# Kernel optimization log

Measured on AMD Instinct MI355X. Metric: run time of the kernel, lower is better.

The kernel has to match this reference:

```python
import jax, jax.numpy as jnp
import numpy as np

B, S, D = 4, 2048, 1024
H = 16
HD = D // H          # 64
HALF = HD // 2       # 32


def _rope(t, cos, sin):
    # t: [B, S, H, HD]; cos/sin: [S, HALF]
    tr = t.reshape(*t.shape[:-1], HALF, 2)
    t0, t1 = tr[..., 0], tr[..., 1]
    c = cos[None, :, None, :]
    s = sin[None, :, None, :]
    out = jnp.stack([t0 * c - t1 * s, t0 * s + t1 * c], axis=-1)
    return out.reshape(t.shape)


def setup_inputs() -> dict:
    key = jax.random.key(0)
    ks = jax.random.split(key, 7)
    x = jax.random.normal(ks[0], (B, S, D), dtype=jnp.float32)
    # rotary tables (theta=10000 convention)
    inv_freq = 1.0 / (10000.0 ** (np.arange(0, HD, 2, dtype=np.float32) / HD))
    angles = np.arange(S, dtype=np.float32)[:, None] * inv_freq[None, :]
    freqs_cos = jnp.asarray(np.cos(angles))
    freqs_sin = jnp.asarray(np.sin(angles))
    scale = 1.0 / np.sqrt(D)
    wq = jax.random.normal(ks[1], (D, D), dtype=jnp.float32) * scale
    wk = jax.random.normal(ks[2], (D, D), dtype=jnp.float32) * scale
    wv = jax.random.normal(ks[3], (D, D), dtype=jnp.float32) * scale
    wo = jax.random.normal(ks[4], (D, D), dtype=jnp.float32) * scale
    return {"x": x, "freqs_cos": freqs_cos, "freqs_sin": freqs_sin,
            "wq": wq, "wk": wk, "wv": wv, "wo": wo}


def reference(x, freqs_cos, freqs_sin, wq, wk, wv, wo):
    b, s, d = x.shape
    q = (x @ wq.T).reshape(b, s, H, HD)
    k = (x @ wk.T).reshape(b, s, H, HD)
    v = (x @ wv.T).reshape(b, s, H, HD)
    q = _rope(q, freqs_cos, freqs_sin)
    k = _rope(k, freqs_cos, freqs_sin)
    # [B, H, S, HD]
    q = q.transpose(0, 2, 1, 3)
    k = k.transpose(0, 2, 1, 3)
    v = v.transpose(0, 2, 1, 3)
    scores = jnp.einsum("bhqd,bhkd->bhqk", q, k) / jnp.sqrt(jnp.float32(HD))
    causal = jnp.tril(jnp.ones((s, s), dtype=bool))
    scores = jnp.where(causal[None, None, :, :], scores, jnp.finfo(scores.dtype).min)
    attn = jax.nn.softmax(scores, axis=-1)
    out = jnp.einsum("bhqk,bhkd->bhqd", attn, v)
    out = out.transpose(0, 2, 1, 3).reshape(b, s, d)
    return out @ wo.T
```

## Files before the change

### kernel.cpp

```cpp
#include <hip/hip_runtime.h>
#include <hip/hip_bf16.h>
#include <cstdint>
#include <cstddef>

#define BB 4
#define SS 2048
#define DD 1024
#define HH 16
#define HDD 64

typedef __bf16 bf16_t;
typedef __bf16 bf16x8 __attribute__((ext_vector_type(8)));
typedef float f32x4 __attribute__((ext_vector_type(4)));
typedef unsigned u32x2 __attribute__((ext_vector_type(2)));

__device__ __forceinline__ unsigned short f2bf(float f) {
    unsigned u = __float_as_uint(f);
    unsigned r = (u + 0x7FFFu + ((u >> 16) & 1u)) >> 16;
    return (unsigned short)r;
}
__device__ __forceinline__ bf16_t f2bf16(float f) {
    return __builtin_bit_cast(bf16_t, f2bf(f));
}
__device__ __forceinline__ bf16x8 cvt8(float4 a, float4 b) {
    bf16x8 r;
    r[0] = f2bf16(a.x); r[1] = f2bf16(a.y);
    r[2] = f2bf16(a.z); r[3] = f2bf16(a.w);
    r[4] = f2bf16(b.x); r[5] = f2bf16(b.y);
    r[6] = f2bf16(b.z); r[7] = f2bf16(b.w);
    return r;
}
__device__ __forceinline__ unsigned cvtpk_bf16(float lo, float hi) {
    unsigned r;
    asm("v_cvt_pk_bf16_f32 %0, %1, %2" : "=v"(r) : "v"(lo), "v"(hi));
    return r;
}
__device__ __forceinline__ float exp2_raw(float x) {
    float r;
    asm("v_exp_f32 %0, %1" : "=v"(r) : "v"(x));
    return r;
}

#define GLL16(gp, lp)                                                          \
    __builtin_amdgcn_global_load_lds(                                          \
        (const __attribute__((address_space(1))) void*)(gp),                   \
        (__attribute__((address_space(3))) void*)(lp), 16, 0, 0)

__global__ __launch_bounds__(256) void cvt1(const float* __restrict__ in,
                                            bf16_t* __restrict__ out) {
    size_t i = (size_t)blockIdx.x * 256 + threadIdx.x;
    const float4* p = (const float4*)in + i * 2;
    *(bf16x8*)(out + i * 8) = cvt8(p[0], p[1]);
}
__global__ __launch_bounds__(256) void cvt4(
    const float* __restrict__ w0, const float* __restrict__ w1,
    const float* __restrict__ w2, const float* __restrict__ w3,
    bf16_t* __restrict__ o0, bf16_t* __restrict__ o1,
    bf16_t* __restrict__ o2, bf16_t* __restrict__ o3) {
    const float* in = blockIdx.y == 0 ? w0 : blockIdx.y == 1 ? w1
                    : blockIdx.y == 2 ? w2 : w3;
    bf16_t* out = blockIdx.y == 0 ? o0 : blockIdx.y == 1 ? o1
                : blockIdx.y == 2 ? o2 : o3;
    size_t i = (size_t)blockIdx.x * 256 + threadIdx.x;
    const float4* p = (const float4*)in + i * 2;
    *(bf16x8*)(out + i * 8) = cvt8(p[0], p[1]);
}

__global__ __launch_bounds__(256, 2) void gemm_qkv(
    const bf16_t* __restrict__ A, const bf16_t* __restrict__ Wall,
    bf16_t* __restrict__ Qb, bf16_t* __restrict__ Kb,
    bf16_t* __restrict__ Vt,
    const float* __restrict__ fcos, const float* __restrict__ fsin,
    float qscale)
{
    constexpr int K = 1024;
    __shared__ alignas(16) bf16_t lA[128 * 64];
    __shared__ alignas(16) bf16_t lB[128 * 64];

    const int tid  = threadIdx.x;
    const int w    = tid >> 6;
    const int lane = tid & 63;
    const int quad = lane >> 4;
    const int l16  = lane & 15;
    const int wm   = w >> 1;
    const int wn   = w & 1;
    const int m0   = blockIdx.y * 128;
    const int n0   = blockIdx.x * 128;
    const int sub  = n0 >> 10;

    f32x4 acc[4][4];
#pragma unroll
    for (int i = 0; i < 4; i++)
#pragma unroll
        for (int j = 0; j < 4; j++) acc[i][j] = (f32x4){0.f, 0.f, 0.f, 0.f};

    const int srow8 = lane >> 3;
    const int slot  = lane & 7;

    for (int k0 = 0; k0 < K; k0 += 64) {
#pragma unroll
        for (int i = 0; i < 4; ++i) {
            int row = w * 32 + i * 8;
            GLL16(A + (size_t)(m0 + row + srow8) * K + k0 + slot * 8,
                  &lA[row * 64]);
            GLL16(Wall + (size_t)(n0 + row + srow8) * K + k0 + slot * 8,
                  &lB[row * 64]);
        }
        __syncthreads();
#pragma unroll
        for (int kk = 0; kk < 2; ++kk) {
            bf16x8 af[4], bfr[4];
#pragma unroll
            for (int mt = 0; mt < 4; ++mt)
                af[mt] = *(const bf16x8*)
                    &lA[(wm * 64 + mt * 16 + l16) * 64 + (kk * 4 + quad) * 8];
#pragma unroll
            for (int nt = 0; nt < 4; ++nt)
                bfr[nt] = *(const bf16x8*)
                    &lB[(wn * 64 + nt * 16 + l16) * 64 + (kk * 4 + quad) * 8];
#pragma unroll
            for (int mt = 0; mt < 4; ++mt)
#pragma unroll
                for (int nt = 0; nt < 4; ++nt)
                    acc[mt][nt] = __builtin_amdgcn_mfma_f32_16x16x32_bf16(
                        af[mt], bfr[nt], acc[mt][nt], 0, 0, 0);
        }
        __syncthreads();
    }

    if (sub < 2) {
        unsigned short* Cu = (unsigned short*)(sub == 0 ? Qb : Kb);
        const float scale = sub == 0 ? qscale : 1.0f;
#pragma unroll
        for (int mt = 0; mt < 4; ++mt) {
#pragma unroll
            for (int nt = 0; nt < 4; ++nt) {
                int col  = (n0 & 1023) + wn * 64 + nt * 16 + l16;
                int h    = col >> 6;
                int d    = col & 63;
                int pidx = d >> 1;
                bool even = (col & 1) == 0;
#pragma unroll
                for (int r = 0; r < 4; ++r) {
                    int m = m0 + wm * 64 + mt * 16 + quad * 4 + r;
                    int b = m >> 11;
                    int s = m & 2047;
                    float v  = acc[mt][nt][r];
                    float p  = __shfl_xor(v, 1);
                    float c  = fcos[s * 32 + pidx];
                    float sn = fsin[s * 32 + pidx];
                    float o  = even ? (v * c - p * sn) : (p * sn + v * c);
                    Cu[(size_t)((b * HH + h) * SS + s) * HDD + d] =
                        f2bf(o * scale);
                }
            }
        }
    } else {
        unsigned short* Cu = (unsigned short*)Vt;
#pragma unroll
        for (int mt = 0; mt < 4; ++mt) {
#pragma unroll
            for (int nt = 0; nt < 4; ++nt) {
                int col = (n0 & 1023) + wn * 64 + nt * 16 + l16;
                int h = col >> 6, d = col & 63;
#pragma unroll
                for (int r = 0; r < 4; ++r) {
                    int m = m0 + wm * 64 + mt * 16 + quad * 4 + r;
                    int b = m >> 11, s = m & 2047;
                    Cu[(size_t)((b * HH + h) * HDD + d) * SS + s] =
                        f2bf(acc[mt][nt][r]);
                }
            }
        }
    }
}

__global__ __launch_bounds__(256, 2) void gemm_out(
    const bf16_t* __restrict__ A, const bf16_t* __restrict__ W,
    float* __restrict__ Cf)
{
    constexpr int K = 1024, N = 1024;
    __shared__ alignas(16) bf16_t lA[128 * 64];
    __shared__ alignas(16) bf16_t lB[128 * 64];

    const int tid  = threadIdx.x;
    const int w    = tid >> 6;
    const int lane = tid & 63;
    const int quad = lane >> 4;
    const int l16  = lane & 15;
    const int wm   = w >> 1;
    const int wn   = w & 1;
    const int m0   = blockIdx.y * 128;
    const int n0   = blockIdx.x * 128;

    f32x4 acc[4][4];
#pragma unroll
    for (int i = 0; i < 4; i++)
#pragma unroll
        for (int j = 0; j < 4; j++) acc[i][j] = (f32x4){0.f, 0.f, 0.f, 0.f};

    const int srow8 = lane >> 3;
    const int slot  = lane & 7;

    for (int k0 = 0; k0 < K; k0 += 64) {
#pragma unroll
        for (int i = 0; i < 4; ++i) {
            int row = w * 32 + i * 8;
            GLL16(A + (size_t)(m0 + row + srow8) * K + k0 + slot * 8,
                  &lA[row * 64]);
            GLL16(W + (size_t)(n0 + row + srow8) * K + k0 + slot * 8,
                  &lB[row * 64]);
        }
        __syncthreads();
#pragma unroll
        for (int kk = 0; kk < 2; ++kk) {
            bf16x8 af[4], bfr[4];
#pragma unroll
            for (int mt = 0; mt < 4; ++mt)
                af[mt] = *(const bf16x8*)
                    &lA[(wm * 64 + mt * 16 + l16) * 64 + (kk * 4 + quad) * 8];
#pragma unroll
            for (int nt = 0; nt < 4; ++nt)
                bfr[nt] = *(const bf16x8*)
                    &lB[(wn * 64 + nt * 16 + l16) * 64 + (kk * 4 + quad) * 8];
#pragma unroll
            for (int mt = 0; mt < 4; ++mt)
#pragma unroll
                for (int nt = 0; nt < 4; ++nt)
                    acc[mt][nt] = __builtin_amdgcn_mfma_f32_16x16x32_bf16(
                        af[mt], bfr[nt], acc[mt][nt], 0, 0, 0);
        }
        __syncthreads();
    }

#pragma unroll
    for (int mt = 0; mt < 4; ++mt) {
        int mrow = m0 + wm * 64 + mt * 16 + quad * 4;
#pragma unroll
        for (int nt = 0; nt < 4; ++nt) {
            int col = n0 + wn * 64 + nt * 16 + l16;
#pragma unroll
            for (int r = 0; r < 4; ++r)
                Cf[(size_t)(mrow + r) * N + col] = acc[mt][nt][r];
        }
    }
}

__global__ __launch_bounds__(256, 2) void attn(
    const bf16_t* __restrict__ Q, const bf16_t* __restrict__ Kt,
    const bf16_t* __restrict__ Vt, bf16_t* __restrict__ O)
{
    __shared__ alignas(16) bf16_t lK[128 * 64];
    __shared__ alignas(16) bf16_t lV[64 * 128];

    const int tid  = threadIdx.x;
    const int w    = tid >> 6;
    const int lane = tid & 63;
    const int quad = lane >> 4;
    const int l16  = lane & 15;

    const int blk  = blockIdx.x;
    const int xcd  = blk & 7;
    const int rest = blk >> 3;
    const int j    = rest & 15;
    const int bh   = ((rest >> 4) << 3) | xcd;
    const int T    = (j & 1) ? (j >> 1) : (15 - (j >> 1));

    const int b = bh >> 4, h = bh & 15;
    unsigned short* Ou = (unsigned short*)O;
    const bf16_t* Qb = Q  + (size_t)bh * SS * HDD;
    const bf16_t* Kb = Kt + (size_t)bh * SS * HDD;
    const bf16_t* Vb = Vt + (size_t)bh * HDD * SS;

    const int q0 = T * 128 + w * 32;
    const int nt128 = T + 1;

    const int krow_l = lane >> 3;
    const int kchk   = lane & 7;
    const int vrow_l = lane >> 4;
    const int vchk   = lane & 15;

    auto stage = [&](int kb2) {
#pragma unroll
        for (int i = 0; i < 4; ++i) {
            int row = w * 32 + i * 8 + krow_l;
            GLL16(Kb + (size_t)(kb2 + row) * HDD + ((kchk ^ (row & 7)) * 8),
                  &lK[(w * 32 + i * 8) * 64]);
        }
#pragma unroll
        for (int i = 0; i < 4; ++i) {
            int row = w * 16 + i * 4 + vrow_l;
            GLL16(Vb + (size_t)row * SS + kb2 + ((vchk ^ (row & 7)) * 8),
                  &lV[(w * 16 + i * 4) * 128]);
        }
    };

    bf16x8 qf[2][2];
#pragma unroll
    for (int qs = 0; qs < 2; ++qs) {
        const bf16_t* qp =
            Qb + (size_t)(q0 + qs * 16 + l16) * HDD + quad * 8;
        qf[qs][0] = *(const bf16x8*)(qp);
        qf[qs][1] = *(const bf16x8*)(qp + 32);
    }

    f32x4 o[2][4];
    float ps[2];
#pragma unroll
    for (int qs = 0; qs < 2; ++qs) {
        ps[qs] = 0.f;
#pragma unroll
        for (int i = 0; i < 4; ++i) o[qs][i] = (f32x4){0.f, 0.f, 0.f, 0.f};
    }

    for (int t = 0; t < nt128; ++t) {
        const int kb2 = t * 128;
        stage(kb2);
        __syncthreads();

        for (int p = 0; p < 2; ++p) {
            const int kbp = kb2 + p * 64;
            if (kbp < q0 + 32) {
                const bool diag = (kbp + 63 > q0);

                bf16x8 kf[4][2];
#pragma unroll
                for (int nt = 0; nt < 4; ++nt) {
                    const int row = p * 64 + nt * 16 + l16;
#pragma unroll
                    for (int hf = 0; hf < 2; ++hf)
                        kf[nt][hf] = *(const bf16x8*)
                            &lK[row * 64 + (((hf * 4 + quad) ^ (row & 7)) * 8)];
                }
                bf16x8 vf[2][4];
#pragma unroll
                for (int kk = 0; kk < 2; ++kk)
#pragma unroll
                    for (int nt = 0; nt < 4; ++nt) {
                        const int row = nt * 16 + l16;
                        vf[kk][nt] = *(const bf16x8*)
                            &lV[row * 128 +
                                ((p * 8 + ((kk * 4 + quad) ^ (row & 7))) * 8)];
                    }

                unsigned pk[4][2][2];
#pragma unroll
                for (int nt = 0; nt < 4; ++nt) {
                    const int krow = kbp + nt * 16 + quad * 4;
#pragma unroll
                    for (int qs = 0; qs < 2; ++qs) {
                        f32x4 s = (f32x4){0.f, 0.f, 0.f, 0.f};
                        s = __builtin_amdgcn_mfma_f32_16x16x32_bf16(
                            kf[nt][0], qf[qs][0], s, 0, 0, 0);
                        s = __builtin_amdgcn_mfma_f32_16x16x32_bf16(
                            kf[nt][1], qf[qs][1], s, 0, 0, 0);
                        if (diag) {
                            const int qcol = q0 + qs * 16 + l16;
#pragma unroll
                            for (int r = 0; r < 4; ++r)
                                if (krow + r > qcol) s[r] = -1e30f;
                        }
                        float ev[4];
#pragma unroll
                        for (int r = 0; r < 4; ++r) {
                            float e = exp2_raw(s[r]);
                            ps[qs] += e;
                            ev[r] = e;
                        }
                        pk[nt][qs][0] = cvtpk_bf16(ev[0], ev[1]);
                        pk[nt][qs][1] = cvtpk_bf16(ev[2], ev[3]);
                    }
                }

#pragma unroll
                for (int kk = 0; kk < 2; ++kk) {
#pragma unroll
                    for (int qs = 0; qs < 2; ++qs) {
                        u32x2 sA = __builtin_amdgcn_permlane32_swap(
                            pk[2 * kk][qs][0], pk[2 * kk + 1][qs][0],
                            false, false);
                        u32x2 sB = __builtin_amdgcn_permlane32_swap(
                            pk[2 * kk][qs][1], pk[2 * kk + 1][qs][1],
                            false, false);
                        u32x2 tA = __builtin_amdgcn_permlane16_swap(
                            sA.x, sA.y, false, false);
                        u32x2 tB = __builtin_amdgcn_permlane16_swap(
                            sB.x, sB.y, false, false);
                        union { unsigned d[4]; bf16x8 v; } pf;
                        pf.d[0] = tA.x;
                        pf.d[1] = tB.x;
                        pf.d[2] = tA.y;
                        pf.d[3] = tB.y;
#pragma unroll
                        for (int nt = 0; nt < 4; ++nt)
                            o[qs][nt] = __builtin_amdgcn_mfma_f32_16x16x32_bf16(
                                pf.v, vf[kk][nt], o[qs][nt], 0, 0, 0);
                    }
                }
            }
        }
        __syncthreads();
    }

#pragma unroll
    for (int qs = 0; qs < 2; ++qs) {
        float tsum = ps[qs];
        tsum += __shfl_xor(tsum, 16);
        tsum += __shfl_xor(tsum, 32);
        float inv[4];
#pragma unroll
        for (int r = 0; r < 4; ++r)
            inv[r] = 1.0f / __shfl(tsum, quad * 4 + r);
#pragma unroll
        for (int nt = 0; nt < 4; ++nt) {
            int d = nt * 16 + l16;
#pragma unroll
            for (int r = 0; r < 4; ++r) {
                int s = q0 + qs * 16 + quad * 4 + r;
                Ou[(size_t)(b * SS + s) * DD + h * HDD + d] =
                    f2bf(o[qs][nt][r] * inv[r]);
            }
        }
    }
}

extern "C" void kernel_launch(void* const* d_in, const int* in_sizes, int n_in,
                              void* d_out, int out_size, void* d_ws,
                              size_t ws_size, hipStream_t stream)
{
    const float* x    = (const float*)d_in[0];
    const float* fcos = (const float*)d_in[1];
    const float* fsin = (const float*)d_in[2];
    const float* wq   = (const float*)d_in[3];
    const float* wk   = (const float*)d_in[4];
    const float* wv   = (const float*)d_in[5];
    const float* wo   = (const float*)d_in[6];

    char* ws = (char*)d_ws;
    const size_t TSZ = (size_t)BB * SS * DD * sizeof(bf16_t);
    const size_t WSZ = (size_t)DD * DD * sizeof(bf16_t);
    bf16_t* Qb  = (bf16_t*)(ws);
    bf16_t* Kb  = (bf16_t*)(ws + TSZ);
    bf16_t* Ob  = (bf16_t*)(ws + 2 * TSZ);
    bf16_t* wb0 = (bf16_t*)(ws + 3 * TSZ);
    bf16_t* wb1 = (bf16_t*)(ws + 3 * TSZ + WSZ);
    bf16_t* wb2 = (bf16_t*)(ws + 3 * TSZ + 2 * WSZ);
    bf16_t* wb3 = (bf16_t*)(ws + 3 * TSZ + 3 * WSZ);
    bf16_t* xb  = (bf16_t*)d_out;
    bf16_t* Vt  = (bf16_t*)((char*)d_out + TSZ);

    dim3 bb(256);
    cvt1<<<dim3(4096), bb, 0, stream>>>(x, xb);
    cvt4<<<dim3(512, 4), bb, 0, stream>>>(wq, wk, wv, wo, wb0, wb1, wb2, wb3);

    const float sscale = 0.125f * 1.44269504088896f;
    gemm_qkv<<<dim3(24, 64), bb, 0, stream>>>(xb, wb0, Qb, Kb, Vt,
                                              fcos, fsin, sscale);
    attn<<<dim3(1024), bb, 0, stream>>>(Qb, Kb, Vt, Ob);
    gemm_out<<<dim3(8, 64), bb, 0, stream>>>(Ob, wb3, (float*)d_out);
}
```

Baseline: 280.1 us.

## Double-buffer K/V tiles and process paired causal q-tiles per attention block

The attention kernel now stages K and V into two LDS buffers, prefetching the next 128-key tile while computing the current one, so there is one barrier per tile instead of two. Each wave handles 64 query rows instead of 32, and each block processes two 256-row query tiles (g and 7-g) in sequence to balance causal work, which cuts the grid from 1024 to 256 blocks. This lets each K/V tile be reused across more queries and hides global load latency. In exchange, LDS use doubles and accumulator and register pressure grow, which may lower occupancy, and 256 blocks may underfill the GPU's compute units.

```diff
diff --git a/kernel.cpp b/kernel.cpp
--- a/kernel.cpp
+++ b/kernel.cpp
@@ -250,8 +250,8 @@
     const bf16_t* __restrict__ Q, const bf16_t* __restrict__ Kt,
     const bf16_t* __restrict__ Vt, bf16_t* __restrict__ O)
 {
-    __shared__ alignas(16) bf16_t lK[128 * 64];
-    __shared__ alignas(16) bf16_t lV[64 * 128];
+    __shared__ alignas(16) bf16_t lK[2][128 * 64];
+    __shared__ alignas(16) bf16_t lV[2][2][64 * 64];
 
     const int tid  = threadIdx.x;
     const int w    = tid >> 6;
@@ -262,9 +262,8 @@
     const int blk  = blockIdx.x;
     const int xcd  = blk & 7;
     const int rest = blk >> 3;
-    const int j    = rest & 15;
-    const int bh   = ((rest >> 4) << 3) | xcd;
-    const int T    = (j & 1) ? (j >> 1) : (15 - (j >> 1));
+    const int g    = rest & 3;
+    const int bh   = ((rest >> 2) << 3) | xcd;
 
     const int b = bh >> 4, h = bh & 15;
     unsigned short* Ou = (unsigned short*)O;
@@ -272,153 +271,163 @@
     const bf16_t* Kb = Kt + (size_t)bh * SS * HDD;
     const bf16_t* Vb = Vt + (size_t)bh * HDD * SS;
 
-    const int q0 = T * 128 + w * 32;
-    const int nt128 = T + 1;
-
-    const int krow_l = lane >> 3;
-    const int kchk   = lane & 7;
-    const int vrow_l = lane >> 4;
-    const int vchk   = lane & 15;
-
-    auto stage = [&](int kb2) {
-#pragma unroll
-        for (int i = 0; i < 4; ++i) {
-            int row = w * 32 + i * 8 + krow_l;
-            GLL16(Kb + (size_t)(kb2 + row) * HDD + ((kchk ^ (row & 7)) * 8),
-                  &lK[(w * 32 + i * 8) * 64]);
-        }
-#pragma unroll
-        for (int i = 0; i < 4; ++i) {
-            int row = w * 16 + i * 4 + vrow_l;
-            GLL16(Vb + (size_t)row * SS + kb2 + ((vchk ^ (row & 7)) * 8),
-                  &lV[(w * 16 + i * 4) * 128]);
-        }
-    };
-
-    bf16x8 qf[2][2];
-#pragma unroll
-    for (int qs = 0; qs < 2; ++qs) {
-        const bf16_t* qp =
-            Qb + (size_t)(q0 + qs * 16 + l16) * HDD + quad * 8;
-        qf[qs][0] = *(const bf16x8*)(qp);
-        qf[qs][1] = *(const bf16x8*)(qp + 32);
-    }
-
-    f32x4 o[2][4];
-    float ps[2];
-#pragma unroll
-    for (int qs = 0; qs < 2; ++qs) {
-        ps[qs] = 0.f;
-#pragma unroll
-        for (int i = 0; i < 4; ++i) o[qs][i] = (f32x4){0.f, 0.f, 0.f, 0.f};
-    }
-
-    for (int t = 0; t < nt128; ++t) {
-        const int kb2 = t * 128;
-        stage(kb2);
+    const int row8 = lane >> 3;
+    const int chk  = lane & 7;
+
+    for (int phase = 0; phase < 2; ++phase) {
+        const int Tp  = phase ? 7 - g : g;
+        const int q0  = Tp * 256 + w * 64;
+        const int nkb = 2 * Tp + 2;
+
+        bf16x8 qf[4][2];
+#pragma unroll
+        for (int qs = 0; qs < 4; ++qs) {
+            const bf16_t* qp =
+                Qb + (size_t)(q0 + qs * 16 + l16) * HDD + quad * 8;
+            qf[qs][0] = *(const bf16x8*)(qp);
+            qf[qs][1] = *(const bf16x8*)(qp + 32);
+        }
+
+        f32x4 o[4][4];
+        float ps[4];
+#pragma unroll
+        for (int qs = 0; qs < 4; ++qs) {
+            ps[qs] = 0.f;
+#pragma unroll
+            for (int i = 0; i < 4; ++i) o[qs][i] = (f32x4){0.f, 0.f, 0.f, 0.f};
+        }
+
+        auto stage = [&](int kb2, int buf) {
+#pragma unroll
+            for (int i = 0; i < 4; ++i) {
+                int rbase = w * 32 + i * 8;
+                int row   = rbase + row8;
+                GLL16(Kb + (size_t)(kb2 + row) * HDD + ((chk ^ (row & 7)) * 8),
+                      &lK[buf][rbase * 64]);
+            }
+#pragma unroll
+            for (int pp = 0; pp < 2; ++pp)
+#pragma unroll
+                for (int i = 0; i < 2; ++i) {
+                    int rbase = w * 16 + i * 8;
+                    int row   = rbase + row8;
+                    GLL16(Vb + (size_t)row * SS + kb2 + pp * 64 +
+                              ((chk ^ (row & 7)) * 8),
+                          &lV[buf][pp][rbase * 64]);
+                }
+        };
+
+        stage(0, 0);
         __syncthreads();
 
-        for (int p = 0; p < 2; ++p) {
-            const int kbp = kb2 + p * 64;
-            if (kbp < q0 + 32) {
-                const bool diag = (kbp + 63 > q0);
-
-                bf16x8 kf[4][2];
-#pragma unroll
-                for (int nt = 0; nt < 4; ++nt) {
-                    const int row = p * 64 + nt * 16 + l16;
-#pragma unroll
-                    for (int hf = 0; hf < 2; ++hf)
-                        kf[nt][hf] = *(const bf16x8*)
-                            &lK[row * 64 + (((hf * 4 + quad) ^ (row & 7)) * 8)];
-                }
-                bf16x8 vf[2][4];
-#pragma unroll
-                for (int kk = 0; kk < 2; ++kk)
+        for (int t = 0; t < nkb; ++t) {
+            const int kb2 = t * 128;
+            const int cur = t & 1;
+            if (t + 1 < nkb) stage(kb2 + 128, cur ^ 1);
+
+#pragma unroll
+            for (int p = 0; p < 2; ++p) {
+                const int kbp = kb2 + p * 64;
+                if (kbp < q0 + 64) {
+                    const bool diag = (kbp + 63 > q0);
+
+                    bf16x8 kf[4][2];
 #pragma unroll
                     for (int nt = 0; nt < 4; ++nt) {
-                        const int row = nt * 16 + l16;
-                        vf[kk][nt] = *(const bf16x8*)
-                            &lV[row * 128 +
-                                ((p * 8 + ((kk * 4 + quad) ^ (row & 7))) * 8)];
+                        const int row = p * 64 + nt * 16 + l16;
+#pragma unroll
+                        for (int hf = 0; hf < 2; ++hf)
+                            kf[nt][hf] = *(const bf16x8*)
+                                &lK[cur][row * 64 +
+                                         (((hf * 4 + quad) ^ (row & 7)) * 8)];
                     }
 
-                unsigned pk[4][2][2];
-#pragma unroll
-                for (int nt = 0; nt < 4; ++nt) {
-                    const int krow = kbp + nt * 16 + quad * 4;
-#pragma unroll
-                    for (int qs = 0; qs < 2; ++qs) {
-                        f32x4 s = (f32x4){0.f, 0.f, 0.f, 0.f};
-                        s = __builtin_amdgcn_mfma_f32_16x16x32_bf16(
-                            kf[nt][0], qf[qs][0], s, 0, 0, 0);
-                        s = __builtin_amdgcn_mfma_f32_16x16x32_bf16(
-                            kf[nt][1], qf[qs][1], s, 0, 0, 0);
-                        if (diag) {
-                            const int qcol = q0 + qs * 16 + l16;
-#pragma unroll
-                            for (int r = 0; r < 4; ++r)
-                                if (krow + r > qcol) s[r] = -1e30f;
+                    unsigned pk[4][4][2];
+#pragma unroll
+                    for (int nt = 0; nt < 4; ++nt) {
+                        const int krow = kbp + nt * 16 + quad * 4;
+#pragma unroll
+                        for (int qs = 0; qs < 4; ++qs) {
+                            f32x4 s = (f32x4){0.f, 0.f, 0.f, 0.f};
+                            s = __builtin_amdgcn_mfma_f32_16x16x32_bf16(
+                                kf[nt][0], qf[qs][0], s, 0, 0, 0);
+                            s = __builtin_amdgcn_mfma_f32_16x16x32_bf16(
+                                kf[nt][1], qf[qs][1], s, 0, 0, 0);
+                            if (diag) {
+                                const int qcol = q0 + qs * 16 + l16;
+#pragma unroll
+                                for (int r = 0; r < 4; ++r)
+                                    if (krow + r > qcol) s[r] = -1e30f;
+                            }
+                            float ev[4];
+#pragma unroll
+                            for (int r = 0; r < 4; ++r) {
+                                float e = exp2_raw(s[r]);
+                                ps[qs] += e;
+                                ev[r] = e;
+                            }
+                            pk[nt][qs][0] = cvtpk_bf16(ev[0], ev[1]);
+                            pk[nt][qs][1] = cvtpk_bf16(ev[2], ev[3]);
                         }
-                        float ev[4];
-#pragma unroll
-                        for (int r = 0; r < 4; ++r) {
-                            float e = exp2_raw(s[r]);
-                            ps[qs] += e;
-                            ev[r] = e;
+                    }
+
+#pragma unroll
+                    for (int kk = 0; kk < 2; ++kk) {
+                        bf16x8 vfk[4];
+#pragma unroll
+                        for (int nt = 0; nt < 4; ++nt) {
+                            const int row = nt * 16 + l16;
+                            vfk[nt] = *(const bf16x8*)
+                                &lV[cur][p][row * 64 +
+                                            (((kk * 4 + quad) ^ (row & 7)) * 8)];
                         }
-                        pk[nt][qs][0] = cvtpk_bf16(ev[0], ev[1]);
-                        pk[nt][qs][1] = cvtpk_bf16(ev[2], ev[3]);
-                    }
-                }
-
-#pragma unroll
-                for (int kk = 0; kk < 2; ++kk) {
-#pragma unroll
-                    for (int qs = 0; qs < 2; ++qs) {
-                        u32x2 sA = __builtin_amdgcn_permlane32_swap(
-                            pk[2 * kk][qs][0], pk[2 * kk + 1][qs][0],
-                            false, false);
-                        u32x2 sB = __builtin_amdgcn_permlane32_swap(
-                            pk[2 * kk][qs][1], pk[2 * kk + 1][qs][1],
-                            false, false);
-                        u32x2 tA = __builtin_amdgcn_permlane16_swap(
-                            sA.x, sA.y, false, false);
-                        u32x2 tB = __builtin_amdgcn_permlane16_swap(
-                            sB.x, sB.y, false, false);
-                        union { unsigned d[4]; bf16x8 v; } pf;
-                        pf.d[0] = tA.x;
-                        pf.d[1] = tB.x;
-                        pf.d[2] = tA.y;
-                        pf.d[3] = tB.y;
-#pragma unroll
-                        for (int nt = 0; nt < 4; ++nt)
-                            o[qs][nt] = __builtin_amdgcn_mfma_f32_16x16x32_bf16(
-                                pf.v, vf[kk][nt], o[qs][nt], 0, 0, 0);
+#pragma unroll
+                        for (int qs = 0; qs < 4; ++qs) {
+                            u32x2 sA = __builtin_amdgcn_permlane32_swap(
+                                pk[2 * kk][qs][0], pk[2 * kk + 1][qs][0],
+                                false, false);
+                            u32x2 sB = __builtin_amdgcn_permlane32_swap(
+                                pk[2 * kk][qs][1], pk[2 * kk + 1][qs][1],
+                                false, false);
+                            u32x2 tA = __builtin_amdgcn_permlane16_swap(
+                                sA.x, sA.y, false, false);
+                            u32x2 tB = __builtin_amdgcn_permlane16_swap(
+                                sB.x, sB.y, false, false);
+                            union { unsigned d[4]; bf16x8 v; } pf;
+                            pf.d[0] = tA.x;
+                            pf.d[1] = tB.x;
+                            pf.d[2] = tA.y;
+                            pf.d[3] = tB.y;
+#pragma unroll
+                            for (int nt = 0; nt < 4; ++nt)
+                                o[qs][nt] =
+                                    __builtin_amdgcn_mfma_f32_16x16x32_bf16(
+                                        pf.v, vfk[nt], o[qs][nt], 0, 0, 0);
+                        }
                     }
                 }
             }
-        }
-        __syncthreads();
-    }
-
-#pragma unroll
-    for (int qs = 0; qs < 2; ++qs) {
-        float tsum = ps[qs];
-        tsum += __shfl_xor(tsum, 16);
-        tsum += __shfl_xor(tsum, 32);
-        float inv[4];
-#pragma unroll
-        for (int r = 0; r < 4; ++r)
-            inv[r] = 1.0f / __shfl(tsum, quad * 4 + r);
-#pragma unroll
-        for (int nt = 0; nt < 4; ++nt) {
-            int d = nt * 16 + l16;
-#pragma unroll
-            for (int r = 0; r < 4; ++r) {
-                int s = q0 + qs * 16 + quad * 4 + r;
-                Ou[(size_t)(b * SS + s) * DD + h * HDD + d] =
-                    f2bf(o[qs][nt][r] * inv[r]);
+            __syncthreads();
+        }
+
+#pragma unroll
+        for (int qs = 0; qs < 4; ++qs) {
+            float tsum = ps[qs];
+            tsum += __shfl_xor(tsum, 16);
+            tsum += __shfl_xor(tsum, 32);
+            float inv[4];
+#pragma unroll
+            for (int r = 0; r < 4; ++r)
+                inv[r] = 1.0f / __shfl(tsum, quad * 4 + r);
+#pragma unroll
+            for (int nt = 0; nt < 4; ++nt) {
+                int d = nt * 16 + l16;
+#pragma unroll
+                for (int r = 0; r < 4; ++r) {
+                    int s = q0 + qs * 16 + quad * 4 + r;
+                    Ou[(size_t)(b * SS + s) * DD + h * HDD + d] =
+                        f2bf(o[qs][nt][r] * inv[r]);
+                }
             }
         }
     }
@@ -456,6 +465,6 @@
     const float sscale = 0.125f * 1.44269504088896f;
     gemm_qkv<<<dim3(24, 64), bb, 0, stream>>>(xb, wb0, Qb, Kb, Vt,
                                               fcos, fsin, sscale);
-    attn<<<dim3(1024), bb, 0, stream>>>(Qb, Kb, Vt, Ob);
+    attn<<<dim3(256), bb, 0, stream>>>(Qb, Kb, Vt, Ob);
     gemm_out<<<dim3(8, 64), bb, 0, stream>>>(Ob, wb3, (float*)d_out);
 }
```

Measured after the change: 278.0 us. Within noise of the previous version (-0.7%).
